# Kernel tuning notes

Measured on AMD Instinct MI355X. Metric: run time of the kernel, lower is better.

Reference implementation:

```python
import jax, jax.numpy as jnp
import numpy as np

GAMMA = 0.99
LAM = 0.95
EPS = 1e-8


def setup_inputs() -> dict:
    key = jax.random.key(0)
    k1, k2, k3 = jax.random.split(key, 3)
    T, N = 2048, 8192
    rewards = jax.random.normal(k1, (T, N), dtype=jnp.float32)
    values = jax.random.normal(k2, (T + 1, N), dtype=jnp.float32)
    dones = jax.random.randint(k3, (T, N), 0, 2, dtype=jnp.int32)
    return {"rewards": rewards, "values": values, "dones": dones}


def reference(rewards, values, dones):
    # rewards: [T, N], values: [T+1, N], dones: [T, N]
    nonterminal = 1.0 - dones.astype(rewards.dtype)        # [T, N]
    # delta_t = r_t + gamma * V_{t+1} * nt_t - V_t
    delta = rewards + GAMMA * values[1:] * nonterminal - values[:-1]
    coef = (GAMMA * LAM) * nonterminal                      # [T, N]

    def step(carry, xs):
        d, c = xs
        a = d + c * carry
        return a, a

    init = jnp.zeros(rewards.shape[1], dtype=rewards.dtype)
    _, advantages = jax.lax.scan(step, init, (delta, coef), reverse=True)
    returns = advantages + values[:-1]
    # torch .std() is unbiased (ddof=1)
    mean = advantages.mean()
    std = advantages.std(ddof=1)
    advantages_norm = (advantages - mean) / (std + EPS)
    return advantages_norm, returns
```

## Files before the change

### kernel.cpp

```cpp
#include <hip/hip_runtime.h>
#include <math.h>

#define GAMMA_ 0.99f
#define GL_ (0.99f * 0.95f)

__global__ __launch_bounds__(256)
void gae_pass1(const float* __restrict__ rw, const float* __restrict__ vv,
               const int* __restrict__ dn,
               float* __restrict__ A, float* __restrict__ B,
               float* __restrict__ Sa, float* __restrict__ Sa2,
               float* __restrict__ SaP, float* __restrict__ SP,
               float* __restrict__ SP2,
               unsigned long long* __restrict__ mask,
               int T, int N, int L)
{
    int n = blockIdx.x * blockDim.x + threadIdx.x;
    int chunk = blockIdx.y;
    if (n >= N) return;
    int s = chunk * L;
    int e = s + L; if (e > T) e = T;
    int idx = chunk * N + n;
    if (s >= T) {
        A[idx] = 0.f; B[idx] = 1.f;
        Sa[idx] = 0.f; Sa2[idx] = 0.f; SaP[idx] = 0.f; SP[idx] = 0.f; SP2[idx] = 0.f;
        mask[idx] = 0ull;
        return;
    }
    float a = 0.f, P = 1.f;
    float sa = 0.f, sa2 = 0.f, saP = 0.f, sP = 0.f, sP2 = 0.f;
    unsigned long long m = 0ull;
    float vnext = vv[(size_t)e * N + n];
    for (int t = e - 1; t >= s; --t) {
        size_t off = (size_t)t * N + n;
        float nt = (dn[off] == 0) ? 1.0f : 0.0f;
        float vc = vv[off];
        float delta = rw[off] + GAMMA_ * vnext * nt - vc;
        float c = GL_ * nt;
        a = delta + c * a;
        P = c * P;
        sa += a; sa2 += a * a; saP += a * P; sP += P; sP2 += P * P;
        m |= ((unsigned long long)(nt != 0.f)) << (t - s);
        vnext = vc;
    }
    A[idx] = a; B[idx] = P;
    Sa[idx] = sa; Sa2[idx] = sa2; SaP[idx] = saP; SP[idx] = sP; SP2[idx] = sP2;
    mask[idx] = m;
}

__global__ __launch_bounds__(256)
void gae_pass2(const float* __restrict__ A, const float* __restrict__ B,
               const float* __restrict__ Sa, const float* __restrict__ Sa2,
               const float* __restrict__ SaP, const float* __restrict__ SP,
               const float* __restrict__ SP2,
               float* __restrict__ carry, double* __restrict__ sums,
               int N, int C)
{
    int n = blockIdx.x * blockDim.x + threadIdx.x;
    double lsum = 0.0, lsq = 0.0;
    if (n < N) {
        float g = 0.f;
        for (int i = C - 1; i >= 0; --i) {
            int idx = i * N + n;
            carry[idx] = g;
            float e = g;
            lsum += (double)(Sa[idx] + SP[idx] * e);
            lsq  += (double)(Sa2[idx] + 2.0f * e * SaP[idx] + (e * e) * SP2[idx]);
            g = A[idx] + B[idx] * g;
        }
    }
    __shared__ double sh[512];
    sh[threadIdx.x] = lsum;
    sh[256 + threadIdx.x] = lsq;
    __syncthreads();
    for (int off = 128; off > 0; off >>= 1) {
        if ((int)threadIdx.x < off) {
            sh[threadIdx.x] += sh[threadIdx.x + off];
            sh[256 + threadIdx.x] += sh[256 + threadIdx.x + off];
        }
        __syncthreads();
    }
    if (threadIdx.x == 0) {
        atomicAdd(&sums[0], sh[0]);
        atomicAdd(&sums[1], sh[256]);
    }
}

__global__ __launch_bounds__(256)
void gae_pass3(const float* __restrict__ rw, const float* __restrict__ vv,
               const unsigned long long* __restrict__ mask,
               const float* __restrict__ carry, const double* __restrict__ sums,
               float* __restrict__ out_adv, float* __restrict__ out_ret,
               int T, int N, int L, double Minv, double Mm1inv)
{
    int n = blockIdx.x * blockDim.x + threadIdx.x;
    int chunk = blockIdx.y;
    if (n >= N) return;
    int s = chunk * L;
    if (s >= T) return;
    int e = s + L; if (e > T) e = T;

    double S = sums[0], S2 = sums[1];
    double meand = S * Minv;
    double vard = (S2 - S * S * Minv) * Mm1inv;
    float mean = (float)meand;
    float inv = (float)(1.0 / (sqrt(vard) + 1e-8));

    int idx = chunk * N + n;
    float a = carry[idx];
    unsigned long long m = mask[idx];
    float vnext = vv[(size_t)e * N + n];
    for (int t = e - 1; t >= s; --t) {
        size_t off = (size_t)t * N + n;
        float nt = (float)((m >> (t - s)) & 1ull);
        float vc = vv[off];
        float delta = rw[off] + GAMMA_ * vnext * nt - vc;
        a = delta + GL_ * nt * a;
        out_adv[off] = (a - mean) * inv;
        out_ret[off] = a + vc;
        vnext = vc;
    }
}

extern "C" void kernel_launch(void* const* d_in, const int* in_sizes, int n_in,
                              void* d_out, int out_size, void* d_ws, size_t ws_size,
                              hipStream_t stream)
{
    const float* rw = (const float*)d_in[0];
    const float* vv = (const float*)d_in[1];
    const int*   dn = (const int*)d_in[2];

    long long TN = in_sizes[0];
    long long VN = in_sizes[1];
    int N = (int)(VN - TN);
    int T = (int)(TN / N);
    int L = 64;
    int C = (T + L - 1) / L;

    char* ws = (char*)d_ws;
    double* sums = (double*)ws;
    size_t cn = (size_t)C * N;
    unsigned long long* mask = (unsigned long long*)(ws + 16);
    float* f   = (float*)(ws + 16 + cn * 8);
    float* A   = f;
    float* B   = f + cn;
    float* Sa  = f + 2 * cn;
    float* Sa2 = f + 3 * cn;
    float* SaP = f + 4 * cn;
    float* SP  = f + 5 * cn;
    float* SP2 = f + 6 * cn;
    float* cry = f + 7 * cn;

    hipMemsetAsync(d_ws, 0, 16, stream);

    dim3 blk(256);
    dim3 g1((N + 255) / 256, C);
    gae_pass1<<<g1, blk, 0, stream>>>(rw, vv, dn, A, B, Sa, Sa2, SaP, SP, SP2,
                                      mask, T, N, L);
    gae_pass2<<<dim3((N + 255) / 256), blk, 0, stream>>>(A, B, Sa, Sa2, SaP, SP,
                                                         SP2, cry, sums, N, C);
    double M = (double)TN;
    gae_pass3<<<g1, blk, 0, stream>>>(rw, vv, mask, cry, sums,
                                      (float*)d_out, (float*)d_out + TN,
                                      T, N, L, 1.0 / M, 1.0 / (M - 1.0));
}
```

Baseline: 349.2 us.

## Vectorize GAE passes with float4, shrink chunks to 32, and use wave-shuffle reduction

Each thread in pass 1 and pass 3 now handles four adjacent columns through float4/int4 loads and stores. The chunk length drops from 64 to 32 so the done-mask fits in a 32-bit word, and the grid gets more chunks along T to keep parallelism after vectorization. Pass 2 runs 64-thread blocks and reduces with wavefront shuffles instead of an LDS tree, at the cost of more atomics. Halving the chunk length doubles the per-chunk summary traffic and lengthens the serial carry loop in pass 2, and the code now assumes N is divisible by 4.

```diff
diff --git a/kernel.cpp b/kernel.cpp
--- a/kernel.cpp
+++ b/kernel.cpp
@@ -3,51 +3,70 @@
 
 #define GAMMA_ 0.99f
 #define GL_ (0.99f * 0.95f)
+#define L_ 32
 
 __global__ __launch_bounds__(256)
-void gae_pass1(const float* __restrict__ rw, const float* __restrict__ vv,
-               const int* __restrict__ dn,
-               float* __restrict__ A, float* __restrict__ B,
-               float* __restrict__ Sa, float* __restrict__ Sa2,
-               float* __restrict__ SaP, float* __restrict__ SP,
-               float* __restrict__ SP2,
-               unsigned long long* __restrict__ mask,
-               int T, int N, int L)
+void gae_pass1(const float4* __restrict__ rw, const float4* __restrict__ vv,
+               const int4* __restrict__ dn,
+               float4* __restrict__ A, float4* __restrict__ B,
+               float4* __restrict__ Sa, float4* __restrict__ Sa2,
+               float4* __restrict__ SaP, float4* __restrict__ SP,
+               float4* __restrict__ SP2, uint4* __restrict__ mask,
+               int T, int N4)
 {
-    int n = blockIdx.x * blockDim.x + threadIdx.x;
+    int q = blockIdx.x * blockDim.x + threadIdx.x;
     int chunk = blockIdx.y;
-    if (n >= N) return;
-    int s = chunk * L;
-    int e = s + L; if (e > T) e = T;
-    int idx = chunk * N + n;
-    if (s >= T) {
-        A[idx] = 0.f; B[idx] = 1.f;
-        Sa[idx] = 0.f; Sa2[idx] = 0.f; SaP[idx] = 0.f; SP[idx] = 0.f; SP2[idx] = 0.f;
-        mask[idx] = 0ull;
-        return;
+    if (q >= N4) return;
+    int s = chunk * L_;
+    int e = s + L_; if (e > T) e = T;
+
+    float a[4] = {0.f,0.f,0.f,0.f}, P[4] = {1.f,1.f,1.f,1.f};
+    float sa[4] = {0.f,0.f,0.f,0.f}, sa2[4] = {0.f,0.f,0.f,0.f};
+    float saP[4] = {0.f,0.f,0.f,0.f}, sP[4] = {0.f,0.f,0.f,0.f};
+    float sP2[4] = {0.f,0.f,0.f,0.f};
+    unsigned mm[4] = {0u,0u,0u,0u};
+
+    float4 vn4 = vv[(size_t)e * N4 + q];
+    float vnext[4] = {vn4.x, vn4.y, vn4.z, vn4.w};
+
+    #pragma unroll 2
+    for (int t = e - 1; t >= s; --t) {
+        size_t off = (size_t)t * N4 + q;
+        float4 r4 = rw[off];
+        int4   d4 = dn[off];
+        float4 v4 = vv[off];
+        float rr[4] = {r4.x, r4.y, r4.z, r4.w};
+        int   dd[4] = {d4.x, d4.y, d4.z, d4.w};
+        float vc[4] = {v4.x, v4.y, v4.z, v4.w};
+        unsigned bit = 1u << (t - s);
+        #pragma unroll
+        for (int j = 0; j < 4; ++j) {
+            float nt = (dd[j] == 0) ? 1.0f : 0.0f;
+            float delta = rr[j] + GAMMA_ * vnext[j] * nt - vc[j];
+            float c = GL_ * nt;
+            a[j] = delta + c * a[j];
+            P[j] = c * P[j];
+            sa[j]  += a[j];
+            sa2[j] += a[j] * a[j];
+            saP[j] += a[j] * P[j];
+            sP[j]  += P[j];
+            sP2[j] += P[j] * P[j];
+            if (dd[j] == 0) mm[j] |= bit;
+            vnext[j] = vc[j];
+        }
     }
-    float a = 0.f, P = 1.f;
-    float sa = 0.f, sa2 = 0.f, saP = 0.f, sP = 0.f, sP2 = 0.f;
-    unsigned long long m = 0ull;
-    float vnext = vv[(size_t)e * N + n];
-    for (int t = e - 1; t >= s; --t) {
-        size_t off = (size_t)t * N + n;
-        float nt = (dn[off] == 0) ? 1.0f : 0.0f;
-        float vc = vv[off];
-        float delta = rw[off] + GAMMA_ * vnext * nt - vc;
-        float c = GL_ * nt;
-        a = delta + c * a;
-        P = c * P;
-        sa += a; sa2 += a * a; saP += a * P; sP += P; sP2 += P * P;
-        m |= ((unsigned long long)(nt != 0.f)) << (t - s);
-        vnext = vc;
-    }
-    A[idx] = a; B[idx] = P;
-    Sa[idx] = sa; Sa2[idx] = sa2; SaP[idx] = saP; SP[idx] = sP; SP2[idx] = sP2;
-    mask[idx] = m;
+    size_t idx = (size_t)chunk * N4 + q;
+    A[idx]   = make_float4(a[0], a[1], a[2], a[3]);
+    B[idx]   = make_float4(P[0], P[1], P[2], P[3]);
+    Sa[idx]  = make_float4(sa[0], sa[1], sa[2], sa[3]);
+    Sa2[idx] = make_float4(sa2[0], sa2[1], sa2[2], sa2[3]);
+    SaP[idx] = make_float4(saP[0], saP[1], saP[2], saP[3]);
+    SP[idx]  = make_float4(sP[0], sP[1], sP[2], sP[3]);
+    SP2[idx] = make_float4(sP2[0], sP2[1], sP2[2], sP2[3]);
+    mask[idx] = make_uint4(mm[0], mm[1], mm[2], mm[3]);
 }
 
-__global__ __launch_bounds__(256)
+__global__ __launch_bounds__(64)
 void gae_pass2(const float* __restrict__ A, const float* __restrict__ B,
                const float* __restrict__ Sa, const float* __restrict__ Sa2,
                const float* __restrict__ SaP, const float* __restrict__ SP,
@@ -68,56 +87,63 @@
             g = A[idx] + B[idx] * g;
         }
     }
-    __shared__ double sh[512];
-    sh[threadIdx.x] = lsum;
-    sh[256 + threadIdx.x] = lsq;
-    __syncthreads();
-    for (int off = 128; off > 0; off >>= 1) {
-        if ((int)threadIdx.x < off) {
-            sh[threadIdx.x] += sh[threadIdx.x + off];
-            sh[256 + threadIdx.x] += sh[256 + threadIdx.x + off];
-        }
-        __syncthreads();
+    for (int off = 32; off > 0; off >>= 1) {
+        lsum += __shfl_down(lsum, off, 64);
+        lsq  += __shfl_down(lsq, off, 64);
     }
-    if (threadIdx.x == 0) {
-        atomicAdd(&sums[0], sh[0]);
-        atomicAdd(&sums[1], sh[256]);
+    if ((threadIdx.x & 63) == 0) {
+        atomicAdd(&sums[0], lsum);
+        atomicAdd(&sums[1], lsq);
     }
 }
 
 __global__ __launch_bounds__(256)
-void gae_pass3(const float* __restrict__ rw, const float* __restrict__ vv,
-               const unsigned long long* __restrict__ mask,
-               const float* __restrict__ carry, const double* __restrict__ sums,
-               float* __restrict__ out_adv, float* __restrict__ out_ret,
-               int T, int N, int L, double Minv, double Mm1inv)
+void gae_pass3(const float4* __restrict__ rw, const float4* __restrict__ vv,
+               const uint4* __restrict__ mask, const float4* __restrict__ carry,
+               const double* __restrict__ sums,
+               float4* __restrict__ out_adv, float4* __restrict__ out_ret,
+               int T, int N4, double Minv, double Mm1inv)
 {
-    int n = blockIdx.x * blockDim.x + threadIdx.x;
+    int q = blockIdx.x * blockDim.x + threadIdx.x;
     int chunk = blockIdx.y;
-    if (n >= N) return;
-    int s = chunk * L;
-    if (s >= T) return;
-    int e = s + L; if (e > T) e = T;
+    if (q >= N4) return;
+    int s = chunk * L_;
+    int e = s + L_; if (e > T) e = T;
 
     double S = sums[0], S2 = sums[1];
-    double meand = S * Minv;
+    float mean = (float)(S * Minv);
     double vard = (S2 - S * S * Minv) * Mm1inv;
-    float mean = (float)meand;
     float inv = (float)(1.0 / (sqrt(vard) + 1e-8));
 
-    int idx = chunk * N + n;
-    float a = carry[idx];
-    unsigned long long m = mask[idx];
-    float vnext = vv[(size_t)e * N + n];
+    size_t idx = (size_t)chunk * N4 + q;
+    float4 c4 = carry[idx];
+    uint4  m4 = mask[idx];
+    float a[4] = {c4.x, c4.y, c4.z, c4.w};
+    unsigned mm[4] = {m4.x, m4.y, m4.z, m4.w};
+
+    float4 vn4 = vv[(size_t)e * N4 + q];
+    float vnext[4] = {vn4.x, vn4.y, vn4.z, vn4.w};
+
+    #pragma unroll 2
     for (int t = e - 1; t >= s; --t) {
-        size_t off = (size_t)t * N + n;
-        float nt = (float)((m >> (t - s)) & 1ull);
-        float vc = vv[off];
-        float delta = rw[off] + GAMMA_ * vnext * nt - vc;
-        a = delta + GL_ * nt * a;
-        out_adv[off] = (a - mean) * inv;
-        out_ret[off] = a + vc;
-        vnext = vc;
+        size_t off = (size_t)t * N4 + q;
+        float4 r4 = rw[off];
+        float4 v4 = vv[off];
+        float rr[4] = {r4.x, r4.y, r4.z, r4.w};
+        float vc[4] = {v4.x, v4.y, v4.z, v4.w};
+        float oa[4], orr[4];
+        unsigned bit = 1u << (t - s);
+        #pragma unroll
+        for (int j = 0; j < 4; ++j) {
+            float nt = (mm[j] & bit) ? 1.0f : 0.0f;
+            float delta = rr[j] + GAMMA_ * vnext[j] * nt - vc[j];
+            a[j] = delta + GL_ * nt * a[j];
+            oa[j]  = (a[j] - mean) * inv;
+            orr[j] = a[j] + vc[j];
+            vnext[j] = vc[j];
+        }
+        out_adv[off] = make_float4(oa[0], oa[1], oa[2], oa[3]);
+        out_ret[off] = make_float4(orr[0], orr[1], orr[2], orr[3]);
     }
 }
 
@@ -133,14 +159,14 @@
     long long VN = in_sizes[1];
     int N = (int)(VN - TN);
     int T = (int)(TN / N);
-    int L = 64;
-    int C = (T + L - 1) / L;
+    int N4 = N / 4;
+    int C = (T + L_ - 1) / L_;
 
     char* ws = (char*)d_ws;
     double* sums = (double*)ws;
     size_t cn = (size_t)C * N;
-    unsigned long long* mask = (unsigned long long*)(ws + 16);
-    float* f   = (float*)(ws + 16 + cn * 8);
+    unsigned* mask = (unsigned*)(ws + 16);
+    float* f   = (float*)(ws + 16 + cn * 4);
     float* A   = f;
     float* B   = f + cn;
     float* Sa  = f + 2 * cn;
@@ -153,13 +179,19 @@
     hipMemsetAsync(d_ws, 0, 16, stream);
 
     dim3 blk(256);
-    dim3 g1((N + 255) / 256, C);
-    gae_pass1<<<g1, blk, 0, stream>>>(rw, vv, dn, A, B, Sa, Sa2, SaP, SP, SP2,
-                                      mask, T, N, L);
-    gae_pass2<<<dim3((N + 255) / 256), blk, 0, stream>>>(A, B, Sa, Sa2, SaP, SP,
-                                                         SP2, cry, sums, N, C);
+    dim3 g1((N4 + 255) / 256, C);
+    gae_pass1<<<g1, blk, 0, stream>>>(
+        (const float4*)rw, (const float4*)vv, (const int4*)dn,
+        (float4*)A, (float4*)B, (float4*)Sa, (float4*)Sa2, (float4*)SaP,
+        (float4*)SP, (float4*)SP2, (uint4*)mask, T, N4);
+
+    gae_pass2<<<dim3((N + 63) / 64), dim3(64), 0, stream>>>(
+        A, B, Sa, Sa2, SaP, SP, SP2, cry, sums, N, C);
+
     double M = (double)TN;
-    gae_pass3<<<g1, blk, 0, stream>>>(rw, vv, mask, cry, sums,
-                                      (float*)d_out, (float*)d_out + TN,
-                                      T, N, L, 1.0 / M, 1.0 / (M - 1.0));
+    gae_pass3<<<g1, blk, 0, stream>>>(
+        (const float4*)rw, (const float4*)vv, (const uint4*)mask,
+        (const float4*)cry, sums,
+        (float4*)d_out, (float4*)((float*)d_out + TN),
+        T, N4, 1.0 / M, 1.0 / (M - 1.0));
 }
```

Result: faster. 329.0 us (-5.8%).
